# Kernel tuning notes

Hardware: AMD Instinct MI355X
Metric: run time of the kernel (lower is better)

The kernel has to match this reference:

```python
import jax, jax.numpy as jnp
import numpy as np

N = 100000   # nodes
E = 1600000  # edges (avg degree 16)
D = 64       # feature dim
STEPS = 3

def setup_inputs() -> dict:
    key = jax.random.key(0)
    ks = jax.random.split(key, 16)
    def rn(i, shape, scale=1.0):
        return jax.random.normal(ks[i], shape, dtype=jnp.float32) * scale
    inp = {
        "nodes": rn(0, (N, D)),
        "edges": rn(1, (E, D)),
        "globals_": rn(2, (1, D)),
        "senders": jax.random.randint(ks[3], (E,), 0, N, dtype=jnp.int32),
        "receivers": jax.random.randint(ks[4], (E,), 0, N, dtype=jnp.int32),
        # edge MLP: in 4*D -> D -> D
        "We1": rn(5, (4 * D, D), (4 * D) ** -0.5),
        "be1": jnp.zeros((D,), jnp.float32),
        "We2": rn(6, (D, D), D ** -0.5),
        "be2": jnp.zeros((D,), jnp.float32),
        # node MLP: in 3*D -> D -> D
        "Wn1": rn(7, (3 * D, D), (3 * D) ** -0.5),
        "bn1": jnp.zeros((D,), jnp.float32),
        "Wn2": rn(8, (D, D), D ** -0.5),
        "bn2": jnp.zeros((D,), jnp.float32),
        # global MLP: in 3*D -> D -> D
        "Wg1": rn(9, (3 * D, D), (3 * D) ** -0.5),
        "bg1": jnp.zeros((D,), jnp.float32),
        "Wg2": rn(10, (D, D), D ** -0.5),
        "bg2": jnp.zeros((D,), jnp.float32),
    }
    return inp

def _mlp(x, W1, b1, W2, b2):
    return jax.nn.relu(x @ W1 + b1) @ W2 + b2

def reference(nodes, edges, globals_, senders, receivers,
              We1, be1, We2, be2, Wn1, bn1, Wn2, bn2, Wg1, bg1, Wg2, bg2):
    g = globals_  # [1, D], single graph
    n_nodes = nodes.shape[0]
    for _ in range(STEPS):
        # --- edge update: gather sender/receiver node feats + broadcast globals ---
        sent = nodes[senders]        # [E, D]
        recv = nodes[receivers]      # [E, D]
        ge = jnp.broadcast_to(g, (edges.shape[0], g.shape[-1]))
        edges = _mlp(jnp.concatenate([edges, sent, recv, ge], axis=-1),
                     We1, be1, We2, be2)  # [E, D]
        # --- aggregate edges to nodes (received messages) ---
        received = jax.ops.segment_sum(edges, receivers, num_segments=n_nodes)
        gn = jnp.broadcast_to(g, (n_nodes, g.shape[-1]))
        nodes = _mlp(jnp.concatenate([nodes, received, gn], axis=-1),
                     Wn1, bn1, Wn2, bn2)  # [N, D]
        # --- aggregate to globals (single graph => full sums) ---
        agg_n = jnp.sum(nodes, axis=0, keepdims=True)  # [1, D]
        agg_e = jnp.sum(edges, axis=0, keepdims=True)  # [1, D]
        g = _mlp(jnp.concatenate([agg_n, agg_e, g], axis=-1),
                 Wg1, bg1, Wg2, bg2)  # [1, D]
    return nodes, edges, g
```

## Files before the change

kernel.cpp:

```cpp
#include <hip/hip_runtime.h>

#define DD 64
typedef unsigned int uint32;
typedef unsigned short ushort16;
typedef short bf16x8 __attribute__((ext_vector_type(8)));
typedef float f32x4 __attribute__((ext_vector_type(4)));

__device__ __forceinline__ ushort16 f2bf(float x) {
    uint32 u = __float_as_uint(x);
    uint32 r = (u + 0x7FFFu + ((u >> 16) & 1u)) >> 16;
    return (ushort16)r;
}
__device__ __forceinline__ float bf2f(ushort16 h) {
    return __uint_as_float(((uint32)h) << 16);
}

__device__ __forceinline__ void split8f(const float4& a, const float4& b, bf16x8& ah, bf16x8& al) {
    float xs[8] = {a.x, a.y, a.z, a.w, b.x, b.y, b.z, b.w};
#pragma unroll
    for (int i = 0; i < 8; ++i) {
        ushort16 hi = f2bf(xs[i]);
        ah[i] = (short)hi;
        al[i] = (short)f2bf(xs[i] - bf2f(hi));
    }
}
__device__ __forceinline__ void unpack8(const uint4& a, const uint4& b, bf16x8& ah, bf16x8& al) {
    uint32 us[8] = {a.x, a.y, a.z, a.w, b.x, b.y, b.z, b.w};
#pragma unroll
    for (int i = 0; i < 8; ++i) {
        ah[i] = (short)(us[i] >> 16);
        al[i] = (short)(us[i] & 0xFFFFu);
    }
}

__device__ __forceinline__ void mfma_ks(const unsigned short* __restrict__ wks, int l,
                                        const bf16x8* ah, const bf16x8* al, f32x4 (*acc)[4]) {
#pragma unroll
    for (int tt = 0; tt < 4; ++tt) {
        bf16x8 bh = *(const bf16x8*)(wks + ((size_t)(tt * 2 + 0) * 64 + l) * 8);
        bf16x8 bl = *(const bf16x8*)(wks + ((size_t)(tt * 2 + 1) * 64 + l) * 8);
#pragma unroll
        for (int m = 0; m < 4; ++m) {
            acc[m][tt] = __builtin_amdgcn_mfma_f32_16x16x32_bf16(ah[m], bh, acc[m][tt], 0, 0, 0);
            acc[m][tt] = __builtin_amdgcn_mfma_f32_16x16x32_bf16(ah[m], bl, acc[m][tt], 0, 0, 0);
            acc[m][tt] = __builtin_amdgcn_mfma_f32_16x16x32_bf16(al[m], bh, acc[m][tt], 0, 0, 0);
        }
    }
}

__device__ __forceinline__ void mfma_ks1(const unsigned short* __restrict__ wks, int l,
                                         bf16x8 ah, bf16x8 al, f32x4* acc) {
#pragma unroll
    for (int tt = 0; tt < 4; ++tt) {
        bf16x8 bh = *(const bf16x8*)(wks + ((size_t)(tt * 2 + 0) * 64 + l) * 8);
        bf16x8 bl = *(const bf16x8*)(wks + ((size_t)(tt * 2 + 1) * 64 + l) * 8);
        acc[tt] = __builtin_amdgcn_mfma_f32_16x16x32_bf16(ah, bh, acc[tt], 0, 0, 0);
        acc[tt] = __builtin_amdgcn_mfma_f32_16x16x32_bf16(ah, bl, acc[tt], 0, 0, 0);
        acc[tt] = __builtin_amdgcn_mfma_f32_16x16x32_bf16(al, bh, acc[tt], 0, 0, 0);
    }
}

__global__ void zero_counts_kernel(int* __restrict__ counts, int N) {
    int i = blockIdx.x * blockDim.x + threadIdx.x;
    if (i < N) counts[i] = 0;
}

__global__ void hist_kernel(const int* __restrict__ recv, int* __restrict__ counts, int E) {
    int i = blockIdx.x * blockDim.x + threadIdx.x;
    if (i < E) atomicAdd(&counts[recv[i]], 1);
}

__global__ __launch_bounds__(1024) void scan_kernel(const int* __restrict__ counts,
                                                    int* __restrict__ offs,
                                                    int* __restrict__ cursor, int N) {
    __shared__ int sm[1024];
    __shared__ int carryS;
    int t = threadIdx.x;
    if (t == 0) carryS = 0;
    __syncthreads();
    for (int base = 0; base < N; base += 4096) {
        int idx = base + t * 4;
        int x0 = (idx + 0 < N) ? counts[idx + 0] : 0;
        int x1 = (idx + 1 < N) ? counts[idx + 1] : 0;
        int x2 = (idx + 2 < N) ? counts[idx + 2] : 0;
        int x3 = (idx + 3 < N) ? counts[idx + 3] : 0;
        int s1 = x0 + x1, s2 = s1 + x2, s3 = s2 + x3;
        sm[t] = s3;
        __syncthreads();
        for (int d = 1; d < 1024; d <<= 1) {
            int v = (t >= d) ? sm[t - d] : 0;
            __syncthreads();
            sm[t] += v;
            __syncthreads();
        }
        int excl = sm[t] - s3 + carryS;
        if (idx < N)     { offs[idx]     = excl;      cursor[idx]     = excl; }
        if (idx + 1 < N) { offs[idx + 1] = excl + x0; cursor[idx + 1] = excl + x0; }
        if (idx + 2 < N) { offs[idx + 2] = excl + s1; cursor[idx + 2] = excl + s1; }
        if (idx + 3 < N) { offs[idx + 3] = excl + s2; cursor[idx + 3] = excl + s2; }
        int chunkTotal = sm[1023];
        __syncthreads();
        if (t == 0) carryS += chunkTotal;
        __syncthreads();
    }
    if (t == 0) offs[N] = carryS;
}

__global__ void scatter_kernel(const int* __restrict__ recv, int* __restrict__ cursor,
                               int* __restrict__ perm, int E) {
    int i = blockIdx.x * blockDim.x + threadIdx.x;
    if (i < E) {
        int p = atomicAdd(&cursor[recv[i]], 1);
        perm[p] = i;
    }
}

__global__ void prep_bias_kernel(const float* __restrict__ g,
                                 const float* __restrict__ We1, const float* __restrict__ be1,
                                 const float* __restrict__ Wn1, const float* __restrict__ bn1,
                                 float* __restrict__ be1e, float* __restrict__ bn1e) {
    int j = threadIdx.x;
    float a = be1[j];
    float b = bn1[j];
    for (int k = 0; k < DD; ++k) {
        float gk = g[k];
        a = fmaf(gk, We1[(192 + k) * DD + j], a);
        b = fmaf(gk, Wn1[(128 + k) * DD + j], b);
    }
    be1e[j] = a;
    bn1e[j] = b;
}

__global__ void prep_nodes_kernel(const float* __restrict__ src, uint32* __restrict__ dst,
                                  int total) {
    int i = blockIdx.x * blockDim.x + threadIdx.x;
    if (i < total) {
        float x = src[i];
        ushort16 hi = f2bf(x);
        ushort16 lo = f2bf(x - bf2f(hi));
        dst[i] = ((uint32)hi << 16) | (uint32)lo;
    }
}

__device__ __forceinline__ void prep_pack(const float* __restrict__ W, int nks,
                                          unsigned short* __restrict__ dst, int tid) {
    if (tid < nks * 2048) {
        int i = tid & 7, lane = (tid >> 3) & 63, tt = (tid >> 9) & 3, ks = tid >> 11;
        int k = ks * 32 + (lane >> 4) * 8 + i;
        int n = tt * 16 + (lane & 15);
        float x = W[k * DD + n];
        ushort16 hi = f2bf(x);
        ushort16 lo = f2bf(x - bf2f(hi));
        dst[(((ks * 4 + tt) * 2 + 0) * 64 + lane) * 8 + i] = hi;
        dst[(((ks * 4 + tt) * 2 + 1) * 64 + lane) * 8 + i] = lo;
    }
}

__global__ void prep_weights_kernel(const float* __restrict__ We1, const float* __restrict__ We2,
                                    const float* __restrict__ Wn1, const float* __restrict__ Wn2,
                                    unsigned short* __restrict__ we1p, unsigned short* __restrict__ we2p,
                                    unsigned short* __restrict__ wn1p, unsigned short* __restrict__ wn2p) {
    int tid = blockIdx.x * blockDim.x + threadIdx.x;
    prep_pack(We1, 6, we1p, tid);
    prep_pack(We2, 2, we2p, tid);
    prep_pack(Wn1, 4, wn1p, tid);
    prep_pack(Wn2, 2, wn2p, tid);
}

__global__ __launch_bounds__(256, 3) void edge_kernel_mfma(
    const float* __restrict__ edges_in, const uint32* __restrict__ nodes_pk,
    const int* __restrict__ senders, const int* __restrict__ receivers,
    const int* __restrict__ perm,
    const unsigned short* __restrict__ w1, const float* __restrict__ b1,
    const unsigned short* __restrict__ w2, const float* __restrict__ b2,
    float* __restrict__ edges_out, float* __restrict__ received,
    float* __restrict__ agg_e, int E)
{
    __shared__ int PE[4][64];
    __shared__ int SID[4][64];
    __shared__ int RID[4][64];
    __shared__ float PS[4][64];
    __shared__ __align__(16) char HB[4][4096];

    const int t = threadIdx.x;
    const int w = t >> 6, l = t & 63;
    const int lm = l & 15, kq = l >> 4;
    const int base = (blockIdx.x << 8) + (w << 6);

    {
        int pos = base + l;
        int pe = perm[min(pos, E - 1)];
        PE[w][l] = pe;
        SID[w][l] = senders[pe];
        RID[w][l] = receivers[pe];
    }

    int pe_m[4], sid_m[4], rid_m[4];
#pragma unroll
    for (int m = 0; m < 4; ++m) {
        pe_m[m]  = PE[w][(m << 4) + lm];
        sid_m[m] = SID[w][(m << 4) + lm];
        rid_m[m] = RID[w][(m << 4) + lm];
    }

    float4 re[4][4];
#pragma unroll
    for (int m = 0; m < 4; ++m) {
        const float* p = edges_in + (size_t)pe_m[m] * DD + kq * 8;
        re[m][0] = *(const float4*)(p);
        re[m][1] = *(const float4*)(p + 4);
        re[m][2] = *(const float4*)(p + 32);
        re[m][3] = *(const float4*)(p + 36);
    }
    uint4 rs[4][4];
#pragma unroll
    for (int m = 0; m < 4; ++m) {
        const uint32* p = nodes_pk + (size_t)sid_m[m] * DD + kq * 8;
        rs[m][0] = *(const uint4*)(p);
        rs[m][1] = *(const uint4*)(p + 4);
        rs[m][2] = *(const uint4*)(p + 32);
        rs[m][3] = *(const uint4*)(p + 36);
    }

    f32x4 acc[4][4];
#pragma unroll
    for (int tt = 0; tt < 4; ++tt) {
        float b = b1[tt * 16 + lm];
#pragma unroll
        for (int m = 0; m < 4; ++m) { acc[m][tt][0] = b; acc[m][tt][1] = b; acc[m][tt][2] = b; acc[m][tt][3] = b; }
    }

#pragma unroll
    for (int ks2 = 0; ks2 < 2; ++ks2) {
        bf16x8 ah[4], al[4];
#pragma unroll
        for (int m = 0; m < 4; ++m) split8f(re[m][ks2 * 2], re[m][ks2 * 2 + 1], ah[m], al[m]);
        mfma_ks(w1 + (size_t)ks2 * 4096, l, ah, al, acc);
    }

    uint4 rr[4][4];
#pragma unroll
    for (int m = 0; m < 4; ++m) {
        const uint32* p = nodes_pk + (size_t)rid_m[m] * DD + kq * 8;
        rr[m][0] = *(const uint4*)(p);
        rr[m][1] = *(const uint4*)(p + 4);
        rr[m][2] = *(const uint4*)(p + 32);
        rr[m][3] = *(const uint4*)(p + 36);
    }

#pragma unroll
    for (int ks2 = 0; ks2 < 2; ++ks2) {
        bf16x8 ah[4], al[4];
#pragma unroll
        for (int m = 0; m < 4; ++m) unpack8(rs[m][ks2 * 2], rs[m][ks2 * 2 + 1], ah[m], al[m]);
        mfma_ks(w1 + (size_t)(2 + ks2) * 4096, l, ah, al, acc);
    }
#pragma unroll
    for (int ks2 = 0; ks2 < 2; ++ks2) {
        bf16x8 ah[4], al[4];
#pragma unroll
        for (int m = 0; m < 4; ++m) unpack8(rr[m][ks2 * 2], rr[m][ks2 * 2 + 1], ah[m], al[m]);
        mfma_ks(w1 + (size_t)(4 + ks2) * 4096, l, ah, al, acc);
    }

    float b2v[4];
#pragma unroll
    for (int tt = 0; tt < 4; ++tt) b2v[tt] = b2[tt * 16 + lm];
    float sreg[4] = {0.f, 0.f, 0.f, 0.f};
    char* hh = &HB[w][0];
    char* hl = &HB[w][2048];

#pragma unroll
    for (int m = 0; m < 4; ++m) {
#pragma unroll
        for (int tt = 0; tt < 4; ++tt)
#pragma unroll
            for (int r = 0; r < 4; ++r) {
                int row = (kq << 2) + r;
                int col = (tt << 4) + lm;
                float hv = fmaxf(acc[m][tt][r], 0.f);
                ushort16 hi = f2bf(hv);
                ushort16 lo = f2bf(hv - bf2f(hi));
                int boff = (row << 7) + ((((col >> 3) ^ (row & 7)) & 7) << 4) + ((col & 7) << 1);
                *(unsigned short*)(hh + boff) = hi;
                *(unsigned short*)(hl + boff) = lo;
            }

        f32x4 acc2[4];
#pragma unroll
        for (int tt = 0; tt < 4; ++tt) { acc2[tt][0] = b2v[tt]; acc2[tt][1] = b2v[tt]; acc2[tt][2] = b2v[tt]; acc2[tt][3] = b2v[tt]; }
#pragma unroll
        for (int ks = 0; ks < 2; ++ks) {
            int boff = (lm << 7) + ((((kq + ks * 4) ^ (lm & 7)) & 7) << 4);
            bf16x8 ah = *(const bf16x8*)(hh + boff);
            bf16x8 al = *(const bf16x8*)(hl + boff);
            mfma_ks1(w2 + (size_t)ks * 4096, l, ah, al, acc2);
        }

#pragma unroll
        for (int tt = 0; tt < 4; ++tt) {
#pragma unroll
            for (int r = 0; r < 4; ++r) {
                int rowp = base + (m << 4) + (kq << 2) + r;
                if (rowp < E) sreg[tt] += acc2[tt][r];
            }
        }

#pragma unroll
        for (int tt = 0; tt < 4; ++tt)
#pragma unroll
            for (int r = 0; r < 4; ++r) {
                int row = (kq << 2) + r;
                int col = (tt << 4) + lm;
                int boff = (row << 8) + ((((col >> 2) ^ (row & 15)) & 15) << 4) + ((col & 3) << 2);
                *(float*)(&HB[w][0] + boff) = acc2[tt][r];
            }

        {
            int rowp = base + (m << 4) + lm;
            float4* dst = (float4*)(edges_out + (size_t)pe_m[m] * DD);
#pragma unroll
            for (int j = 0; j < 4; ++j) {
                int fc = kq + (j << 2);
                int boff = (lm << 8) + (((fc ^ (lm & 15)) & 15) << 4);
                float4 v = *(float4*)(&HB[w][0] + boff);
                if (rowp < E) dst[fc] = v;
            }
        }

        {
            float run = 0.f;
#pragma unroll
            for (int r = 0; r < 16; ++r) {
                int rowp = base + (m << 4) + r;
                if (rowp < E) {
                    int boff = (r << 8) + ((((l >> 2) ^ (r & 15)) & 15) << 4) + ((l & 3) << 2);
                    float v = *(const float*)(&HB[w][0] + boff);
                    int rid = RID[w][(m << 4) + r];
                    run += v;
                    bool flush;
                    if (r == 15) flush = true;
                    else flush = (rowp + 1 >= E) || (RID[w][(m << 4) + r + 1] != rid);
                    if (flush) {
                        atomicAdd(&received[(size_t)rid * DD + l], run);
                        run = 0.f;
                    }
                }
            }
        }
    }

#pragma unroll
    for (int tt = 0; tt < 4; ++tt) {
        float s = sreg[tt];
        s += __shfl_xor(s, 16, 64);
        s += __shfl_xor(s, 32, 64);
        if (l < 16) PS[w][tt * 16 + l] = s;
    }
    __syncthreads();
    if (t < 64) {
        float s = PS[0][t] + PS[1][t] + PS[2][t] + PS[3][t];
        atomicAdd(agg_e + t, s);
    }
}

__global__ __launch_bounds__(256, 2) void node_kernel_mfma(
    const uint32* __restrict__ nodes_pk, const float* __restrict__ received,
    const unsigned short* __restrict__ w1, const float* __restrict__ b1,
    const unsigned short* __restrict__ w2, const float* __restrict__ b2,
    float* __restrict__ nodes_out, float* __restrict__ agg_n, int N)
{
    __shared__ unsigned short HB[4][4][2][1024];
    __shared__ float PS[4][64];

    const int t = threadIdx.x;
    const int w = t >> 6, l = t & 63;
    const int lm = l & 15, kq = l >> 4;
    const int base = (blockIdx.x << 8) + (w << 6);

    int gi[4];
#pragma unroll
    for (int m = 0; m < 4; ++m) gi[m] = min(base + (m << 4) + lm, N - 1);

    uint4 rn[4][4];
#pragma unroll
    for (int m = 0; m < 4; ++m) {
        const uint32* p = nodes_pk + (size_t)gi[m] * DD + kq * 8;
        rn[m][0] = *(const uint4*)(p);
        rn[m][1] = *(const uint4*)(p + 4);
        rn[m][2] = *(const uint4*)(p + 32);
        rn[m][3] = *(const uint4*)(p + 36);
    }
    float4 rc[4][4];
#pragma unroll
    for (int m = 0; m < 4; ++m) {
        const float* p = received + (size_t)gi[m] * DD + kq * 8;
        rc[m][0] = *(const float4*)(p);
        rc[m][1] = *(const float4*)(p + 4);
        rc[m][2] = *(const float4*)(p + 32);
        rc[m][3] = *(const float4*)(p + 36);
    }

    f32x4 acc[4][4];
#pragma unroll
    for (int tt = 0; tt < 4; ++tt) {
        float b = b1[tt * 16 + lm];
#pragma unroll
        for (int m = 0; m < 4; ++m) { acc[m][tt][0] = b; acc[m][tt][1] = b; acc[m][tt][2] = b; acc[m][tt][3] = b; }
    }

#pragma unroll
    for (int ks2 = 0; ks2 < 2; ++ks2) {
        bf16x8 ah[4], al[4];
#pragma unroll
        for (int m = 0; m < 4; ++m) unpack8(rn[m][ks2 * 2], rn[m][ks2 * 2 + 1], ah[m], al[m]);
        mfma_ks(w1 + (size_t)ks2 * 4096, l, ah, al, acc);
    }
#pragma unroll
    for (int ks2 = 0; ks2 < 2; ++ks2) {
        bf16x8 ah[4], al[4];
#pragma unroll
        for (int m = 0; m < 4; ++m) split8f(rc[m][ks2 * 2], rc[m][ks2 * 2 + 1], ah[m], al[m]);
        mfma_ks(w1 + (size_t)(2 + ks2) * 4096, l, ah, al, acc);
    }

#pragma unroll
    for (int m = 0; m < 4; ++m) {
        char* hh = (char*)&HB[w][m][0][0];
        char* hl = (char*)&HB[w][m][1][0];
#pragma unroll
        for (int tt = 0; tt < 4; ++tt)
#pragma unroll
            for (int r = 0; r < 4; ++r) {
                int row = (kq << 2) + r;
                int col = (tt << 4) + lm;
                float hv = fmaxf(acc[m][tt][r], 0.f);
                ushort16 hi = f2bf(hv);
                ushort16 lo = f2bf(hv - bf2f(hi));
                int boff = (row << 7) + ((((col >> 3) ^ (row & 7)) & 7) << 4) + ((col & 7) << 1);
                *(unsigned short*)(hh + boff) = hi;
                *(unsigned short*)(hl + boff) = lo;
            }
    }

    f32x4 acc2[4][4];
#pragma unroll
    for (int tt = 0; tt < 4; ++tt) {
        float b = b2[tt * 16 + lm];
#pragma unroll
        for (int m = 0; m < 4; ++m) { acc2[m][tt][0] = b; acc2[m][tt][1] = b; acc2[m][tt][2] = b; acc2[m][tt][3] = b; }
    }
#pragma unroll
    for (int ks = 0; ks < 2; ++ks) {
        bf16x8 ah[4], al[4];
#pragma unroll
        for (int m = 0; m < 4; ++m) {
            int boff = (lm << 7) + ((((kq + ks * 4) ^ (lm & 7)) & 7) << 4);
            ah[m] = *(const bf16x8*)((char*)&HB[w][m][0][0] + boff);
            al[m] = *(const bf16x8*)((char*)&HB[w][m][1][0] + boff);
        }
        mfma_ks(w2 + (size_t)ks * 4096, l, ah, al, acc2);
    }

#pragma unroll
    for (int tt = 0; tt < 4; ++tt) {
        float s = 0.f;
#pragma unroll
        for (int m = 0; m < 4; ++m)
#pragma unroll
            for (int r = 0; r < 4; ++r) {
                int rowg = base + (m << 4) + (kq << 2) + r;
                if (rowg < N) s += acc2[m][tt][r];
            }
        s += __shfl_xor(s, 16, 64);
        s += __shfl_xor(s, 32, 64);
        if (l < 16) PS[w][tt * 16 + l] = s;
    }

    char* CW = (char*)&HB[w][0][0][0];
#pragma unroll
    for (int m = 0; m < 4; ++m)
#pragma unroll
        for (int tt = 0; tt < 4; ++tt)
#pragma unroll
            for (int r = 0; r < 4; ++r) {
                int row = (kq << 2) + r;
                int col = (tt << 4) + lm;
                int boff = (row << 8) + ((((col >> 2) ^ (row & 15)) & 15) << 4) + ((col & 3) << 2);
                *(float*)(CW + m * 4096 + boff) = acc2[m][tt][r];
            }
#pragma unroll
    for (int m = 0; m < 4; ++m) {
        int rowg = base + (m << 4) + lm;
        float4* dst = (float4*)(nodes_out + (size_t)rowg * DD);
#pragma unroll
        for (int j = 0; j < 4; ++j) {
            int fc = kq + (j << 2);
            int boff = (lm << 8) + (((fc ^ (lm & 15)) & 15) << 4);
            float4 v = *(float4*)(CW + m * 4096 + boff);
            if (rowg < N) dst[fc] = v;
        }
    }

    __syncthreads();
    if (t < 64) {
        float s = PS[0][t] + PS[1][t] + PS[2][t] + PS[3][t];
        atomicAdd(agg_n + t, s);
    }
}

__global__ void global_kernel(const float* __restrict__ agg_n, const float* __restrict__ agg_e,
                              const float* __restrict__ g_in,
                              const float* __restrict__ Wg1, const float* __restrict__ bg1,
                              const float* __restrict__ Wg2, const float* __restrict__ bg2,
                              float* __restrict__ g_out)
{
    __shared__ float h[64];
    int j = threadIdx.x;
    float a = bg1[j];
    for (int k = 0; k < DD; ++k) a = fmaf(agg_n[k], Wg1[k * DD + j], a);
    for (int k = 0; k < DD; ++k) a = fmaf(agg_e[k], Wg1[(64 + k) * DD + j], a);
    for (int k = 0; k < DD; ++k) a = fmaf(g_in[k],  Wg1[(128 + k) * DD + j], a);
    h[j] = fmaxf(a, 0.f);
    __syncthreads();
    float o = bg2[j];
    for (int k = 0; k < DD; ++k) o = fmaf(h[k], Wg2[k * DD + j], o);
    g_out[j] = o;
}

extern "C" void kernel_launch(void* const* d_in, const int* in_sizes, int n_in,
                              void* d_out, int out_size, void* d_ws, size_t ws_size,
                              hipStream_t stream) {
    const float* nodes0 = (const float*)d_in[0];
    const float* edges0 = (const float*)d_in[1];
    const float* g0     = (const float*)d_in[2];
    const int* senders   = (const int*)d_in[3];
    const int* receivers = (const int*)d_in[4];
    const float* We1 = (const float*)d_in[5];
    const float* be1 = (const float*)d_in[6];
    const float* We2 = (const float*)d_in[7];
    const float* be2 = (const float*)d_in[8];
    const float* Wn1 = (const float*)d_in[9];
    const float* bn1 = (const float*)d_in[10];
    const float* Wn2 = (const float*)d_in[11];
    const float* bn2 = (const float*)d_in[12];
    const float* Wg1 = (const float*)d_in[13];
    const float* bg1 = (const float*)d_in[14];
    const float* Wg2 = (const float*)d_in[15];
    const float* bg2 = (const float*)d_in[16];

    const int N = in_sizes[0] / DD;
    const int E = in_sizes[1] / DD;

    float* out_nodes = (float*)d_out;
    float* out_edges = out_nodes + (size_t)N * DD;
    float* out_g     = out_edges + (size_t)E * DD;

    float* ws = (float*)d_ws;
    float* received = ws;
    float* aggs = received + (size_t)N * DD;
    float* agg_n = aggs;
    float* agg_e = aggs + 64;
    float* b1e   = aggs + 128;
    float* b1n   = aggs + 192;
    float* g1    = aggs + 256;
    float* g2    = aggs + 320;
    int* counts = (int*)(aggs + 512);
    int* offs   = counts + N;
    int* cursor = offs + N + 4;
    int* perm   = cursor + N;
    uint32* nodes_pk = (uint32*)(perm + E);
    unsigned short* we1p = (unsigned short*)(nodes_pk + (size_t)N * DD);
    unsigned short* we2p = we1p + 24576;
    unsigned short* wn1p = we2p + 8192;
    unsigned short* wn2p = wn1p + 16384;

    const int eblocks = (E + 255) / 256;
    const int nblocks = (N + 255) / 256;

    zero_counts_kernel<<<(N + 255) / 256, 256, 0, stream>>>(counts, N);
    hist_kernel<<<(E + 255) / 256, 256, 0, stream>>>(receivers, counts, E);
    scan_kernel<<<1, 1024, 0, stream>>>(counts, offs, cursor, N);
    scatter_kernel<<<(E + 255) / 256, 256, 0, stream>>>(receivers, cursor, perm, E);
    prep_weights_kernel<<<48, 256, 0, stream>>>(We1, We2, Wn1, Wn2, we1p, we2p, wn1p, wn2p);

    for (int s = 0; s < 3; ++s) {
        const float* nsrc = (s == 0) ? nodes0 : out_nodes;
        const float* esrc = (s == 0) ? edges0 : out_edges;
        const float* gin  = (s == 0) ? g0 : ((s == 1) ? g1 : g2);
        float* gout       = (s == 2) ? out_g : ((s == 0) ? g1 : g2);

        hipMemsetAsync(received, 0, ((size_t)N * DD + 128) * sizeof(float), stream);
        prep_bias_kernel<<<1, 64, 0, stream>>>(gin, We1, be1, Wn1, bn1, b1e, b1n);
        prep_nodes_kernel<<<(N * DD + 255) / 256, 256, 0, stream>>>(nsrc, nodes_pk, N * DD);
        edge_kernel_mfma<<<eblocks, 256, 0, stream>>>(esrc, nodes_pk, senders, receivers, perm,
                                                      we1p, b1e, we2p, be2,
                                                      out_edges, received, agg_e, E);
        node_kernel_mfma<<<nblocks, 256, 0, stream>>>(nodes_pk, received, wn1p, b1n, wn2p, bn2,
                                                      out_nodes, agg_n, N);
        global_kernel<<<1, 64, 0, stream>>>(agg_n, agg_e, gin, Wg1, bg1, Wg2, bg2, gout);
    }
}
```

Measured before the change: 1.992 ms.

## Keep intermediate edge features in bf16 and fuse node packing into node kernel

Result: slower. 2.046 ms (+2.7%).

```diff
diff --git a/kernel.cpp b/kernel.cpp
--- a/kernel.cpp
+++ b/kernel.cpp
@@ -14,6 +14,11 @@
 __device__ __forceinline__ float bf2f(ushort16 h) {
     return __uint_as_float(((uint32)h) << 16);
 }
+__device__ __forceinline__ uint32 packsplit(float x) {
+    ushort16 hi = f2bf(x);
+    ushort16 lo = f2bf(x - bf2f(hi));
+    return ((uint32)hi << 16) | (uint32)lo;
+}
 
 __device__ __forceinline__ void split8f(const float4& a, const float4& b, bf16x8& ah, bf16x8& al) {
     float xs[8] = {a.x, a.y, a.z, a.w, b.x, b.y, b.z, b.w};
@@ -47,7 +52,19 @@
         }
     }
 }
-
+__device__ __forceinline__ void mfma_ks_hi(const unsigned short* __restrict__ wks, int l,
+                                           const bf16x8* ah, f32x4 (*acc)[4]) {
+#pragma unroll
+    for (int tt = 0; tt < 4; ++tt) {
+        bf16x8 bh = *(const bf16x8*)(wks + ((size_t)(tt * 2 + 0) * 64 + l) * 8);
+        bf16x8 bl = *(const bf16x8*)(wks + ((size_t)(tt * 2 + 1) * 64 + l) * 8);
+#pragma unroll
+        for (int m = 0; m < 4; ++m) {
+            acc[m][tt] = __builtin_amdgcn_mfma_f32_16x16x32_bf16(ah[m], bh, acc[m][tt], 0, 0, 0);
+            acc[m][tt] = __builtin_amdgcn_mfma_f32_16x16x32_bf16(ah[m], bl, acc[m][tt], 0, 0, 0);
+        }
+    }
+}
 __device__ __forceinline__ void mfma_ks1(const unsigned short* __restrict__ wks, int l,
                                          bf16x8 ah, bf16x8 al, f32x4* acc) {
 #pragma unroll
@@ -64,12 +81,10 @@
     int i = blockIdx.x * blockDim.x + threadIdx.x;
     if (i < N) counts[i] = 0;
 }
-
 __global__ void hist_kernel(const int* __restrict__ recv, int* __restrict__ counts, int E) {
     int i = blockIdx.x * blockDim.x + threadIdx.x;
     if (i < E) atomicAdd(&counts[recv[i]], 1);
 }
-
 __global__ __launch_bounds__(1024) void scan_kernel(const int* __restrict__ counts,
                                                     int* __restrict__ offs,
                                                     int* __restrict__ cursor, int N) {
@@ -105,7 +120,6 @@
     }
     if (t == 0) offs[N] = carryS;
 }
-
 __global__ void scatter_kernel(const int* __restrict__ recv, int* __restrict__ cursor,
                                int* __restrict__ perm, int E) {
     int i = blockIdx.x * blockDim.x + threadIdx.x;
@@ -134,12 +148,7 @@
 __global__ void prep_nodes_kernel(const float* __restrict__ src, uint32* __restrict__ dst,
                                   int total) {
     int i = blockIdx.x * blockDim.x + threadIdx.x;
-    if (i < total) {
-        float x = src[i];
-        ushort16 hi = f2bf(x);
-        ushort16 lo = f2bf(x - bf2f(hi));
-        dst[i] = ((uint32)hi << 16) | (uint32)lo;
-    }
+    if (i < total) dst[i] = packsplit(src[i]);
 }
 
 __device__ __forceinline__ void prep_pack(const float* __restrict__ W, int nks,
@@ -155,7 +164,6 @@
         dst[(((ks * 4 + tt) * 2 + 1) * 64 + lane) * 8 + i] = lo;
     }
 }
-
 __global__ void prep_weights_kernel(const float* __restrict__ We1, const float* __restrict__ We2,
                                     const float* __restrict__ Wn1, const float* __restrict__ Wn2,
                                     unsigned short* __restrict__ we1p, unsigned short* __restrict__ we2p,
@@ -167,14 +175,16 @@
     prep_pack(Wn2, 2, wn2p, tid);
 }
 
-__global__ __launch_bounds__(256, 3) void edge_kernel_mfma(
-    const float* __restrict__ edges_in, const uint32* __restrict__ nodes_pk,
+template<int IN_BF, int OUT_F32>
+__global__ __launch_bounds__(256, 3) void edge_kernel_t(
+    const float* __restrict__ edges_f32, const unsigned short* __restrict__ edges_bf,
+    const uint32* __restrict__ nodes_pk,
     const int* __restrict__ senders, const int* __restrict__ receivers,
     const int* __restrict__ perm,
     const unsigned short* __restrict__ w1, const float* __restrict__ b1,
     const unsigned short* __restrict__ w2, const float* __restrict__ b2,
-    float* __restrict__ edges_out, float* __restrict__ received,
-    float* __restrict__ agg_e, int E)
+    float* __restrict__ eout_f32, unsigned short* __restrict__ eout_bf,
+    float* __restrict__ received, float* __restrict__ agg_e, int E)
 {
     __shared__ int PE[4][64];
     __shared__ int SID[4][64];
@@ -204,13 +214,24 @@
     }
 
     float4 re[4][4];
-#pragma unroll
-    for (int m = 0; m < 4; ++m) {
-        const float* p = edges_in + (size_t)pe_m[m] * DD + kq * 8;
-        re[m][0] = *(const float4*)(p);
-        re[m][1] = *(const float4*)(p + 4);
-        re[m][2] = *(const float4*)(p + 32);
-        re[m][3] = *(const float4*)(p + 36);
+    uint4 rbe[4][2];
+    if (IN_BF) {
+#pragma unroll
+        for (int m = 0; m < 4; ++m) {
+            int row = min(base + (m << 4) + lm, E - 1);
+            const unsigned short* p = edges_bf + (size_t)row * DD;
+            rbe[m][0] = *(const uint4*)(p + kq * 8);
+            rbe[m][1] = *(const uint4*)(p + 32 + kq * 8);
+        }
+    } else {
+#pragma unroll
+        for (int m = 0; m < 4; ++m) {
+            const float* p = edges_f32 + (size_t)pe_m[m] * DD + kq * 8;
+            re[m][0] = *(const float4*)(p);
+            re[m][1] = *(const float4*)(p + 4);
+            re[m][2] = *(const float4*)(p + 32);
+            re[m][3] = *(const float4*)(p + 36);
+        }
     }
     uint4 rs[4][4];
 #pragma unroll
@@ -230,12 +251,22 @@
         for (int m = 0; m < 4; ++m) { acc[m][tt][0] = b; acc[m][tt][1] = b; acc[m][tt][2] = b; acc[m][tt][3] = b; }
     }
 
-#pragma unroll
-    for (int ks2 = 0; ks2 < 2; ++ks2) {
-        bf16x8 ah[4], al[4];
-#pragma unroll
-        for (int m = 0; m < 4; ++m) split8f(re[m][ks2 * 2], re[m][ks2 * 2 + 1], ah[m], al[m]);
-        mfma_ks(w1 + (size_t)ks2 * 4096, l, ah, al, acc);
+    if (IN_BF) {
+#pragma unroll
+        for (int ks2 = 0; ks2 < 2; ++ks2) {
+            bf16x8 ah[4];
+#pragma unroll
+            for (int m = 0; m < 4; ++m) ah[m] = *(bf16x8*)&rbe[m][ks2];
+            mfma_ks_hi(w1 + (size_t)ks2 * 4096, l, ah, acc);
+        }
+    } else {
+#pragma unroll
+        for (int ks2 = 0; ks2 < 2; ++ks2) {
+            bf16x8 ah[4], al[4];
+#pragma unroll
+            for (int m = 0; m < 4; ++m) split8f(re[m][ks2 * 2], re[m][ks2 * 2 + 1], ah[m], al[m]);
+            mfma_ks(w1 + (size_t)ks2 * 4096, l, ah, al, acc);
+        }
     }
 
     uint4 rr[4][4];
@@ -298,13 +329,12 @@
         }
 
 #pragma unroll
-        for (int tt = 0; tt < 4; ++tt) {
+        for (int tt = 0; tt < 4; ++tt)
 #pragma unroll
             for (int r = 0; r < 4; ++r) {
                 int rowp = base + (m << 4) + (kq << 2) + r;
                 if (rowp < E) sreg[tt] += acc2[tt][r];
             }
-        }
 
 #pragma unroll
         for (int tt = 0; tt < 4; ++tt)
@@ -318,13 +348,31 @@
 
         {
             int rowp = base + (m << 4) + lm;
-            float4* dst = (float4*)(edges_out + (size_t)pe_m[m] * DD);
-#pragma unroll
-            for (int j = 0; j < 4; ++j) {
-                int fc = kq + (j << 2);
-                int boff = (lm << 8) + (((fc ^ (lm & 15)) & 15) << 4);
-                float4 v = *(float4*)(&HB[w][0] + boff);
-                if (rowp < E) dst[fc] = v;
+            float4 vv[4];
+#pragma unroll
+            for (int jj = 0; jj < 4; ++jj) {
+                int slot = (4 * kq + jj) ^ (lm & 15);
+                vv[jj] = *(float4*)(&HB[w][0] + (lm << 8) + (slot << 4));
+            }
+            if (rowp < E) {
+                if (OUT_F32) {
+                    float4* dst = (float4*)(eout_f32 + (size_t)pe_m[m] * DD);
+#pragma unroll
+                    for (int jj = 0; jj < 4; ++jj) dst[kq * 4 + jj] = vv[jj];
+                } else {
+                    uint4 o0, o1;
+                    o0.x = (uint32)f2bf(vv[0].x) | ((uint32)f2bf(vv[0].y) << 16);
+                    o0.y = (uint32)f2bf(vv[0].z) | ((uint32)f2bf(vv[0].w) << 16);
+                    o0.z = (uint32)f2bf(vv[1].x) | ((uint32)f2bf(vv[1].y) << 16);
+                    o0.w = (uint32)f2bf(vv[1].z) | ((uint32)f2bf(vv[1].w) << 16);
+                    o1.x = (uint32)f2bf(vv[2].x) | ((uint32)f2bf(vv[2].y) << 16);
+                    o1.y = (uint32)f2bf(vv[2].z) | ((uint32)f2bf(vv[2].w) << 16);
+                    o1.z = (uint32)f2bf(vv[3].x) | ((uint32)f2bf(vv[3].y) << 16);
+                    o1.w = (uint32)f2bf(vv[3].z) | ((uint32)f2bf(vv[3].w) << 16);
+                    unsigned short* dst = eout_bf + (size_t)rowp * DD + kq * 16;
+                    *(uint4*)(dst) = o0;
+                    *(uint4*)(dst + 8) = o1;
+                }
             }
         }
 
@@ -368,7 +416,8 @@
     const uint32* __restrict__ nodes_pk, const float* __restrict__ received,
     const unsigned short* __restrict__ w1, const float* __restrict__ b1,
     const unsigned short* __restrict__ w2, const float* __restrict__ b2,
-    float* __restrict__ nodes_out, float* __restrict__ agg_n, int N)
+    float* __restrict__ nodes_out, uint32* __restrict__ nodes_pk_out, int write_pk,
+    float* __restrict__ agg_n, int N)
 {
     __shared__ unsigned short HB[4][4][2][1024];
     __shared__ float PS[4][64];
@@ -492,13 +541,28 @@
 #pragma unroll
     for (int m = 0; m < 4; ++m) {
         int rowg = base + (m << 4) + lm;
-        float4* dst = (float4*)(nodes_out + (size_t)rowg * DD);
-#pragma unroll
-        for (int j = 0; j < 4; ++j) {
-            int fc = kq + (j << 2);
-            int boff = (lm << 8) + (((fc ^ (lm & 15)) & 15) << 4);
-            float4 v = *(float4*)(CW + m * 4096 + boff);
-            if (rowg < N) dst[fc] = v;
+        float4 vv[4];
+#pragma unroll
+        for (int jj = 0; jj < 4; ++jj) {
+            int slot = (4 * kq + jj) ^ (lm & 15);
+            vv[jj] = *(float4*)(CW + m * 4096 + (lm << 8) + (slot << 4));
+        }
+        if (rowg < N) {
+            float4* dst = (float4*)(nodes_out + (size_t)rowg * DD);
+#pragma unroll
+            for (int jj = 0; jj < 4; ++jj) dst[kq * 4 + jj] = vv[jj];
+            if (write_pk) {
+                uint32* pdst = nodes_pk_out + (size_t)rowg * DD + kq * 16;
+#pragma unroll
+                for (int jj = 0; jj < 4; ++jj) {
+                    uint4 o;
+                    o.x = packsplit(vv[jj].x);
+                    o.y = packsplit(vv[jj].y);
+                    o.z = packsplit(vv[jj].z);
+                    o.w = packsplit(vv[jj].w);
+                    *(uint4*)(pdst + jj * 4) = o;
+                }
+            }
         }
     }
 
@@ -574,6 +638,10 @@
     unsigned short* we2p = we1p + 24576;
     unsigned short* wn1p = we2p + 8192;
     unsigned short* wn2p = wn1p + 16384;
+    unsigned short* edges_bf = wn2p + 8192;
+
+    size_t need = (size_t)((char*)(edges_bf + (size_t)E * DD) - (char*)d_ws);
+    const bool use_bf = (ws_size >= need);
 
     const int eblocks = (E + 255) / 256;
     const int nblocks = (N + 255) / 256;
@@ -583,21 +651,41 @@
     scan_kernel<<<1, 1024, 0, stream>>>(counts, offs, cursor, N);
     scatter_kernel<<<(E + 255) / 256, 256, 0, stream>>>(receivers, cursor, perm, E);
     prep_weights_kernel<<<48, 256, 0, stream>>>(We1, We2, Wn1, Wn2, we1p, we2p, wn1p, wn2p);
+    prep_nodes_kernel<<<(N * DD + 255) / 256, 256, 0, stream>>>(nodes0, nodes_pk, N * DD);
 
     for (int s = 0; s < 3; ++s) {
-        const float* nsrc = (s == 0) ? nodes0 : out_nodes;
-        const float* esrc = (s == 0) ? edges0 : out_edges;
+        const float* esrc_f32 = (s == 0) ? edges0 : out_edges;
         const float* gin  = (s == 0) ? g0 : ((s == 1) ? g1 : g2);
         float* gout       = (s == 2) ? out_g : ((s == 0) ? g1 : g2);
+        const bool in_bf  = use_bf && (s > 0);
+        const bool out_f32 = (!use_bf) || (s == 2);
 
         hipMemsetAsync(received, 0, ((size_t)N * DD + 128) * sizeof(float), stream);
         prep_bias_kernel<<<1, 64, 0, stream>>>(gin, We1, be1, Wn1, bn1, b1e, b1n);
-        prep_nodes_kernel<<<(N * DD + 255) / 256, 256, 0, stream>>>(nsrc, nodes_pk, N * DD);
-        edge_kernel_mfma<<<eblocks, 256, 0, stream>>>(esrc, nodes_pk, senders, receivers, perm,
-                                                      we1p, b1e, we2p, be2,
-                                                      out_edges, received, agg_e, E);
+
+        if (in_bf) {
+            if (out_f32)
+                edge_kernel_t<1, 1><<<eblocks, 256, 0, stream>>>(esrc_f32, edges_bf, nodes_pk,
+                    senders, receivers, perm, we1p, b1e, we2p, be2,
+                    out_edges, edges_bf, received, agg_e, E);
+            else
+                edge_kernel_t<1, 0><<<eblocks, 256, 0, stream>>>(esrc_f32, edges_bf, nodes_pk,
+                    senders, receivers, perm, we1p, b1e, we2p, be2,
+                    out_edges, edges_bf, received, agg_e, E);
+        } else {
+            if (out_f32)
+                edge_kernel_t<0, 1><<<eblocks, 256, 0, stream>>>(esrc_f32, edges_bf, nodes_pk,
+                    senders, receivers, perm, we1p, b1e, we2p, be2,
+                    out_edges, edges_bf, received, agg_e, E);
+            else
+                edge_kernel_t<0, 0><<<eblocks, 256, 0, stream>>>(esrc_f32, edges_bf, nodes_pk,
+                    senders, receivers, perm, we1p, b1e, we2p, be2,
+                    out_edges, edges_bf, received, agg_e, E);
+        }
+
         node_kernel_mfma<<<nblocks, 256, 0, stream>>>(nodes_pk, received, wn1p, b1n, wn2p, bn2,
-                                                      out_nodes, agg_n, N);
+                                                      out_nodes, nodes_pk, (s < 2) ? 1 : 0,
+                                                      agg_n, N);
         global_kernel<<<1, 64, 0, stream>>>(agg_n, agg_e, gin, Wg1, bg1, Wg2, bg2, gout);
     }
 }
```
